# Performance work log

Hardware: AMD Instinct MI355X
Metric: run time of the kernel (lower is better)

The kernel has to match this reference:

```python
import jax, jax.numpy as jnp
import numpy as np

D_MODEL = 2048
N_HEADS = 16
HEAD_DIM = D_MODEL // N_HEADS


def setup_inputs() -> dict:
    key = jax.random.key(0)
    ks = jax.random.split(key, 6)
    B, T = 4, 2048
    scale = 1.0 / np.sqrt(D_MODEL)
    x = jax.random.normal(ks[0], (B, T, D_MODEL), dtype=jnp.float32)
    wq = jax.random.normal(ks[1], (D_MODEL, D_MODEL), dtype=jnp.float32) * scale
    wk = jax.random.normal(ks[2], (D_MODEL, D_MODEL), dtype=jnp.float32) * scale
    wv = jax.random.normal(ks[3], (D_MODEL, D_MODEL), dtype=jnp.float32) * scale
    wo = jax.random.normal(ks[4], (D_MODEL, D_MODEL), dtype=jnp.float32) * scale
    bo = jnp.zeros((D_MODEL,), dtype=jnp.float32)
    return {"x": x, "wq": wq, "wk": wk, "wv": wv, "wo": wo, "bo": bo}


def reference(x, wq, wk, wv, wo, bo):
    B, T, C = x.shape
    H, Dh = N_HEADS, HEAD_DIM
    # torch nn.Linear: y = x @ W.T
    q = (x @ wq.T).reshape(B, T, H, Dh).transpose(0, 2, 1, 3)  # (B,H,T,Dh)
    k = (x @ wk.T).reshape(B, T, H, Dh).transpose(0, 2, 1, 3)
    v = (x @ wv.T).reshape(B, T, H, Dh).transpose(0, 2, 1, 3)
    scores = jnp.einsum('bhqd,bhkd->bhqk', q, k) / np.sqrt(Dh).astype(np.float32)
    attn = jax.nn.softmax(scores, axis=-1)  # no causal mask in source
    out = jnp.einsum('bhqk,bhkd->bhqd', attn, v)
    out = out.transpose(0, 2, 1, 3).reshape(B, T, C)
    return out @ wo.T + bo
```

## Files before the change

kernel.cpp:

```cpp
#include <hip/hip_runtime.h>
#include <hip/hip_bf16.h>
#include <math.h>

typedef __attribute__((ext_vector_type(8))) __bf16 bf16x8;
typedef __attribute__((ext_vector_type(4))) float floatx4;

__device__ inline unsigned short f2u(float f) {
  __hip_bfloat16 h = __float2bfloat16(f);
  unsigned short u;
  __builtin_memcpy(&u, &h, 2);
  return u;
}

__device__ inline floatx4 mfma16(bf16x8 a, bf16x8 b, floatx4 c) {
  return __builtin_amdgcn_mfma_f32_16x16x32_bf16(a, b, c, 0, 0, 0);
}

__device__ inline void gload_lds16(const unsigned short* g, unsigned short* l) {
  __builtin_amdgcn_global_load_lds(
      (__attribute__((address_space(1))) void*)g,
      (__attribute__((address_space(3))) void*)l,
      16, 0, 0);
}

__global__ __launch_bounds__(256) void castk(const float* __restrict__ in,
                                             unsigned short* __restrict__ out,
                                             int n4, float scale) {
  int i = blockIdx.x * 256 + threadIdx.x;
  if (i >= n4) return;
  const float4 v = reinterpret_cast<const float4*>(in)[i];
  ushort4 o;
  o.x = f2u(v.x * scale);
  o.y = f2u(v.y * scale);
  o.z = f2u(v.z * scale);
  o.w = f2u(v.w * scale);
  reinterpret_cast<ushort4*>(out)[i] = o;
}

__global__ __launch_bounds__(256) void castw4(const float* __restrict__ wq,
                                              const float* __restrict__ wk,
                                              const float* __restrict__ wv,
                                              const float* __restrict__ wo,
                                              unsigned short* __restrict__ oq,
                                              unsigned short* __restrict__ ok,
                                              unsigned short* __restrict__ ov,
                                              unsigned short* __restrict__ oo,
                                              float qscale) {
  const int tensor = blockIdx.x >> 12;
  const int i = (blockIdx.x & 4095) * 256 + threadIdx.x;
  const float* in = tensor == 0 ? wq : tensor == 1 ? wk : tensor == 2 ? wv : wo;
  unsigned short* out = tensor == 0 ? oq : tensor == 1 ? ok : tensor == 2 ? ov : oo;
  const float s = tensor == 0 ? qscale : 1.0f;
  const float4 v = reinterpret_cast<const float4*>(in)[i];
  ushort4 o;
  o.x = f2u(v.x * s);
  o.y = f2u(v.y * s);
  o.z = f2u(v.z * s);
  o.w = f2u(v.w * s);
  reinterpret_cast<ushort4*>(out)[i] = o;
}

template <int OUT>
__global__ __launch_bounds__(512, 2)
void gemm256(const unsigned short* __restrict__ A,
             const unsigned short* __restrict__ B,
             unsigned short* __restrict__ Cb,
             float* __restrict__ Cf,
             const float* __restrict__ bias,
             int M, int N, int K) {
  extern __shared__ unsigned short lds[];
  const int t = threadIdx.x;
  const int w = t >> 6;
  const int l = t & 63;
  const int wm = w >> 2;
  const int wn = w & 3;
  const int fr = l & 15;
  const int fkb = l >> 4;
  const int key = fr & 7;
  const int sslot = (l & 7) ^ (l >> 3);

  const int m0 = blockIdx.y * 256;
  const int n0 = blockIdx.x * 256;
  const int T = K >> 6;

  auto stage = [&](const unsigned short* G, int rb, int kt2, int h, int ldsbase) {
    const int d2 = kt2 & 1;
    const int rt = h * 128 + w * 16 + (l >> 3);
    const unsigned short* s0 = G + (size_t)(rb + rt) * K + kt2 * 64 + sslot * 8;
    unsigned short* dst = lds + ldsbase + d2 * 16384 + h * 8192 + w * 1024;
    gload_lds16(s0, dst);
    gload_lds16(s0 + (size_t)8 * K, dst + 512);
  };

  floatx4 acc[8][4];
#pragma unroll
  for (int m = 0; m < 8; m++)
#pragma unroll
    for (int n = 0; n < 4; n++) acc[m][n] = (floatx4){0.f, 0.f, 0.f, 0.f};

  stage(A, m0, 0, 0, 0);
  stage(A, m0, 0, 1, 0);
  stage(B, n0, 0, 0, 32768);
  stage(B, n0, 0, 1, 32768);
  if (1 < T) {
    stage(B, n0, 1, 0, 32768);
    stage(B, n0, 1, 1, 32768);
    asm volatile("s_waitcnt vmcnt(4)" ::: "memory");
  } else {
    asm volatile("s_waitcnt vmcnt(0)" ::: "memory");
  }
  __builtin_amdgcn_s_barrier();

#define GPHASE(q, STAGE_STMT)                                               \
  {                                                                         \
    bf16x8 a00 = *reinterpret_cast<const bf16x8*>(                          \
        Ab + (wm * 128 + (2 * (q)) * 16 + fr) * 64 + ((fkb ^ key)) * 8);    \
    bf16x8 a01 = *reinterpret_cast<const bf16x8*>(                          \
        Ab + (wm * 128 + (2 * (q)) * 16 + fr) * 64 + (((4 + fkb) ^ key)) * 8); \
    bf16x8 a10 = *reinterpret_cast<const bf16x8*>(                          \
        Ab + (wm * 128 + (2 * (q) + 1) * 16 + fr) * 64 + ((fkb ^ key)) * 8);\
    bf16x8 a11 = *reinterpret_cast<const bf16x8*>(                          \
        Ab + (wm * 128 + (2 * (q) + 1) * 16 + fr) * 64 + (((4 + fkb) ^ key)) * 8); \
    STAGE_STMT;                                                             \
    __builtin_amdgcn_s_barrier();                                           \
    asm volatile("s_waitcnt lgkmcnt(0)");                                   \
    __builtin_amdgcn_s_setprio(1);                                          \
    _Pragma("unroll")                                                       \
    for (int n = 0; n < 4; n++) {                                           \
      acc[2 * (q)][n] = mfma16(a00, bfr[0][n], acc[2 * (q)][n]);            \
      acc[2 * (q)][n] = mfma16(a01, bfr[1][n], acc[2 * (q)][n]);            \
      acc[2 * (q) + 1][n] = mfma16(a10, bfr[0][n], acc[2 * (q) + 1][n]);    \
      acc[2 * (q) + 1][n] = mfma16(a11, bfr[1][n], acc[2 * (q) + 1][n]);    \
    }                                                                       \
    __builtin_amdgcn_s_setprio(0);                                          \
    __builtin_amdgcn_s_barrier();                                           \
  }

  for (int kt = 0; kt < T; ++kt) {
    const int d = kt & 1;
    const unsigned short* Ab = lds + d * 16384;
    const unsigned short* Bb = lds + 32768 + d * 16384;

    bf16x8 bfr[2][4];
#pragma unroll
    for (int kk = 0; kk < 2; kk++)
#pragma unroll
      for (int n = 0; n < 4; n++)
        bfr[kk][n] = *reinterpret_cast<const bf16x8*>(
            Bb + (wn * 64 + n * 16 + fr) * 64 + (((kk * 4 + fkb) ^ key)) * 8);

    GPHASE(0, if (kt + 1 < T) stage(A, m0, kt + 1, 0, 0));
    GPHASE(1, if (kt + 1 < T) stage(A, m0, kt + 1, 1, 0));
    GPHASE(2, if (kt + 2 < T) stage(B, n0, kt + 2, 0, 32768));
    GPHASE(3, {
      if (kt + 2 < T) {
        stage(B, n0, kt + 2, 1, 32768);
        asm volatile("s_waitcnt vmcnt(4)" ::: "memory");
      } else {
        asm volatile("s_waitcnt vmcnt(0)" ::: "memory");
      }
    });
  }
#undef GPHASE

  const int er = (l >> 4) * 4;
  const int ec = l & 15;
#pragma unroll
  for (int m = 0; m < 8; m++) {
#pragma unroll
    for (int n = 0; n < 4; n++) {
      const int col = n0 + wn * 64 + n * 16 + ec;
      if (OUT == 2) {
        const int hv = col >> 7, dh = col & 127;
        const int row0 = m0 + wm * 128 + m * 16 + er;
        const int bb = row0 >> 11;
        const int t0 = row0 & 2047;
        unsigned short* vp =
            Cb + (((size_t)(bb * 16 + hv)) * 128 + dh) * 2048 + t0;
#pragma unroll
        for (int r = 0; r < 4; r++) vp[r] = f2u(acc[m][n][r]);
      } else {
#pragma unroll
        for (int r = 0; r < 4; r++) {
          const int row = m0 + wm * 128 + m * 16 + er + r;
          if (OUT == 1) {
            Cf[(size_t)row * N + col] = acc[m][n][r] + bias[col];
          } else {
            Cb[(size_t)row * N + col] = f2u(acc[m][n][r]);
          }
        }
      }
    }
  }
}

__global__ __launch_bounds__(256, 2)
void attn_kernel(const unsigned short* __restrict__ Y2,
                 const unsigned short* __restrict__ Vtg,
                 unsigned short* __restrict__ att) {
  __shared__ unsigned short Kt[64 * 128];
  __shared__ unsigned short Vt[128 * 64];
  __shared__ unsigned short Pl[4][32 * 72];

  const int t = threadIdx.x;
  const int w = t >> 6;
  const int l = t & 63;
  const int bid = blockIdx.x;
  const int bh = bid & 63;
  const int qt = bid >> 6;
  const int b = bh >> 4;
  const int h = bh & 15;

  const size_t ybase = (size_t)b * 2048 * 4096 + (size_t)h * 128;
  const unsigned short* Qp = Y2 + ybase;
  const unsigned short* Kp = Y2 + ybase + 2048;
  const unsigned short* Vp = Vtg + (size_t)bh * 128 * 2048;

  const int fr = l & 15;
  const int fkb = l >> 4;
  const int key = fr & 7;

  const int ksr = t >> 4;
  const int ksl = (t & 15) ^ (ksr & 7);
  const unsigned short* Ksrc = Kp + (size_t)ksr * 4096 + ksl * 8;

  const int vsr = t >> 3;
  const int vsl = (t & 7) ^ (vsr & 7);
  const unsigned short* Vsrc = Vp + (size_t)vsr * 2048 + vsl * 8;

  bf16x8 qf[2][4];
#pragma unroll
  for (int i = 0; i < 2; i++)
#pragma unroll
    for (int kk = 0; kk < 4; kk++)
      qf[i][kk] = *reinterpret_cast<const bf16x8*>(
          &Qp[(size_t)(qt * 128 + w * 32 + i * 16 + fr) * 4096 + kk * 32 + fkb * 8]);

  floatx4 oacc[2][8];
#pragma unroll
  for (int i = 0; i < 2; i++)
#pragma unroll
    for (int nt = 0; nt < 8; nt++) oacc[i][nt] = (floatx4){0.f, 0.f, 0.f, 0.f};
  float mrun[2][4], lrun[2][4];
#pragma unroll
  for (int i = 0; i < 2; i++)
#pragma unroll
    for (int r = 0; r < 4; r++) {
      mrun[i][r] = -INFINITY;
      lrun[i][r] = 0.f;
    }

  unsigned short* Pw = &Pl[w][0];

#pragma unroll
  for (int c = 0; c < 4; c++)
    gload_lds16(Ksrc + (size_t)c * 16 * 4096, &Kt[c * 2048 + w * 512]);
#pragma unroll
  for (int c = 0; c < 4; c++)
    gload_lds16(Vsrc + (size_t)c * 32 * 2048, &Vt[c * 2048 + w * 512]);
  __syncthreads();

  for (int kv = 0; kv < 2048; kv += 64) {
    floatx4 sacc[2][4];
#pragma unroll
    for (int i = 0; i < 2; i++)
#pragma unroll
      for (int nt = 0; nt < 4; nt++) sacc[i][nt] = (floatx4){0.f, 0.f, 0.f, 0.f};
#pragma unroll
    for (int nt = 0; nt < 4; nt++) {
#pragma unroll
      for (int kk = 0; kk < 4; kk++) {
        bf16x8 kf = *reinterpret_cast<const bf16x8*>(
            &Kt[((nt * 16 + fr) * 16 + ((kk * 4 + fkb) ^ key)) * 8]);
        sacc[0][nt] = mfma16(qf[0][kk], kf, sacc[0][nt]);
        sacc[1][nt] = mfma16(qf[1][kk], kf, sacc[1][nt]);
      }
    }

#pragma unroll
    for (int i = 0; i < 2; i++) {
#pragma unroll
      for (int r = 0; r < 4; r++) {
        float s0 = sacc[i][0][r], s1 = sacc[i][1][r];
        float s2 = sacc[i][2][r], s3 = sacc[i][3][r];
        float mx = fmaxf(fmaxf(s0, s1), fmaxf(s2, s3));
        mx = fmaxf(mx, __shfl_xor(mx, 1));
        mx = fmaxf(mx, __shfl_xor(mx, 2));
        mx = fmaxf(mx, __shfl_xor(mx, 4));
        mx = fmaxf(mx, __shfl_xor(mx, 8));
        if (mx > mrun[i][r] + 8.0f) {
          float alpha = __expf(mrun[i][r] - mx);
          mrun[i][r] = mx;
          lrun[i][r] *= alpha;
#pragma unroll
          for (int nt = 0; nt < 8; nt++) oacc[i][nt][r] *= alpha;
        }
        const float m = mrun[i][r];
        float p0 = __expf(s0 - m);
        float p1 = __expf(s1 - m);
        float p2 = __expf(s2 - m);
        float p3 = __expf(s3 - m);
        float ps = (p0 + p1) + (p2 + p3);
        ps += __shfl_xor(ps, 1);
        ps += __shfl_xor(ps, 2);
        ps += __shfl_xor(ps, 4);
        ps += __shfl_xor(ps, 8);
        lrun[i][r] += ps;
        const int pr = i * 16 + fkb * 4 + r;
        Pw[pr * 72 + fr] = f2u(p0);
        Pw[pr * 72 + 16 + fr] = f2u(p1);
        Pw[pr * 72 + 32 + fr] = f2u(p2);
        Pw[pr * 72 + 48 + fr] = f2u(p3);
      }
    }

    __syncthreads();

    if (kv + 64 < 2048) {
#pragma unroll
      for (int c = 0; c < 4; c++)
        gload_lds16(Ksrc + (size_t)(kv + 64 + c * 16) * 4096,
                    &Kt[c * 2048 + w * 512]);
    }

    bf16x8 pf[2][2];
#pragma unroll
    for (int i = 0; i < 2; i++) {
      pf[i][0] = *reinterpret_cast<const bf16x8*>(&Pw[(i * 16 + fr) * 72 + fkb * 8]);
      pf[i][1] = *reinterpret_cast<const bf16x8*>(&Pw[(i * 16 + fr) * 72 + 32 + fkb * 8]);
    }
#pragma unroll
    for (int nt = 0; nt < 8; nt++) {
      const unsigned short* vr = &Vt[(nt * 16 + fr) * 64];
      bf16x8 vf0 = *reinterpret_cast<const bf16x8*>(vr + (fkb ^ key) * 8);
      bf16x8 vf1 = *reinterpret_cast<const bf16x8*>(vr + ((fkb + 4) ^ key) * 8);
#pragma unroll
      for (int i = 0; i < 2; i++) {
        oacc[i][nt] = mfma16(pf[i][0], vf0, oacc[i][nt]);
        oacc[i][nt] = mfma16(pf[i][1], vf1, oacc[i][nt]);
      }
    }

    __syncthreads();

    if (kv + 64 < 2048) {
#pragma unroll
      for (int c = 0; c < 4; c++)
        gload_lds16(Vsrc + (size_t)c * 32 * 2048 + (kv + 64),
                    &Vt[c * 2048 + w * 512]);
    }
  }

#pragma unroll
  for (int i = 0; i < 2; i++) {
#pragma unroll
    for (int r = 0; r < 4; r++) {
      const float inv = 1.0f / lrun[i][r];
      const int row = qt * 128 + w * 32 + i * 16 + fkb * 4 + r;
      unsigned short* op = att + ((size_t)b * 2048 + row) * 2048 + h * 128 + fr;
#pragma unroll
      for (int nt = 0; nt < 8; nt++) op[nt * 16] = f2u(oacc[i][nt][r] * inv);
    }
  }
}

extern "C" void kernel_launch(void* const* d_in, const int* in_sizes, int n_in,
                              void* d_out, int out_size, void* d_ws, size_t ws_size,
                              hipStream_t stream) {
  const float* x = (const float*)d_in[0];
  const float* wq = (const float*)d_in[1];
  const float* wk = (const float*)d_in[2];
  const float* wv = (const float*)d_in[3];
  const float* wo = (const float*)d_in[4];
  const float* bo = (const float*)d_in[5];

  unsigned short* ws = (unsigned short*)d_ws;
  unsigned short* x16 = ws;
  unsigned short* wqkv16 = x16 + 16777216;
  unsigned short* wo16 = wqkv16 + 12582912;
  unsigned short* Y2 = wo16 + 4194304;
  unsigned short* Vtg = Y2 + 33554432;
  unsigned short* att16 = Vtg + 16777216;

  const float sscale = 0.08838834764831845f;

  hipFuncSetAttribute(reinterpret_cast<const void*>(gemm256<0>),
                      hipFuncAttributeMaxDynamicSharedMemorySize, 131072);
  hipFuncSetAttribute(reinterpret_cast<const void*>(gemm256<1>),
                      hipFuncAttributeMaxDynamicSharedMemorySize, 131072);
  hipFuncSetAttribute(reinterpret_cast<const void*>(gemm256<2>),
                      hipFuncAttributeMaxDynamicSharedMemorySize, 131072);

  castk<<<16384, 256, 0, stream>>>(x, x16, 4194304, 1.0f);
  castw4<<<16384, 256, 0, stream>>>(wq, wk, wv, wo,
                                    wqkv16, wqkv16 + 4194304,
                                    wqkv16 + 8388608, wo16, sscale);

  dim3 gqk(16, 32);
  gemm256<0><<<gqk, 512, 131072, stream>>>(x16, wqkv16, Y2, nullptr, nullptr,
                                           8192, 4096, 2048);
  dim3 gv(8, 32);
  gemm256<2><<<gv, 512, 131072, stream>>>(x16, wqkv16 + 8388608, Vtg, nullptr,
                                          nullptr, 8192, 2048, 2048);

  attn_kernel<<<1024, 256, 0, stream>>>(Y2, Vtg, att16);

  dim3 go(8, 32);
  gemm256<1><<<go, 512, 131072, stream>>>(att16, wo16, nullptr, (float*)d_out,
                                          bo, 8192, 2048, 2048);
}
```

Baseline: 542.0 us.

## Enlarge attention blocks to 8 waves and streamline online softmax with exp2

The attention kernel now runs 512-thread blocks, each covering 256 query rows. Each K/V tile staged in LDS therefore serves twice as many queries, and LDS moves to dynamic shared memory. The softmax switches to exp2 by folding log2(e) into the Q weight scale. Rescaling becomes a wave-uniform lazy check, and the per-row sum cross-lane reduction is deferred to the epilogue, cutting shuffles and exp calls per tile. The tighter launch bounds (512,4) may cap registers per thread and cause spills, and the larger block halves the grid size.

Result: slower. 920.7 us (+69.9%).

```diff
diff --git a/kernel.cpp b/kernel.cpp
--- a/kernel.cpp
+++ b/kernel.cpp
@@ -194,13 +194,14 @@
   }
 }
 
-__global__ __launch_bounds__(256, 2)
+__global__ __launch_bounds__(512, 4)
 void attn_kernel(const unsigned short* __restrict__ Y2,
                  const unsigned short* __restrict__ Vtg,
                  unsigned short* __restrict__ att) {
-  __shared__ unsigned short Kt[64 * 128];
-  __shared__ unsigned short Vt[128 * 64];
-  __shared__ unsigned short Pl[4][32 * 72];
+  extern __shared__ unsigned short smem[];
+  unsigned short* Kt = smem;
+  unsigned short* Vt = smem + 8192;
+  unsigned short* Pw = smem + 16384 + (threadIdx.x >> 6) * 2304;
 
   const int t = threadIdx.x;
   const int w = t >> 6;
@@ -223,7 +224,6 @@
   const int ksr = t >> 4;
   const int ksl = (t & 15) ^ (ksr & 7);
   const unsigned short* Ksrc = Kp + (size_t)ksr * 4096 + ksl * 8;
-
   const int vsr = t >> 3;
   const int vsl = (t & 7) ^ (vsr & 7);
   const unsigned short* Vsrc = Vp + (size_t)vsr * 2048 + vsl * 8;
@@ -234,30 +234,28 @@
 #pragma unroll
     for (int kk = 0; kk < 4; kk++)
       qf[i][kk] = *reinterpret_cast<const bf16x8*>(
-          &Qp[(size_t)(qt * 128 + w * 32 + i * 16 + fr) * 4096 + kk * 32 + fkb * 8]);
+          &Qp[(size_t)(qt * 256 + w * 32 + i * 16 + fr) * 4096 + kk * 32 + fkb * 8]);
 
   floatx4 oacc[2][8];
 #pragma unroll
   for (int i = 0; i < 2; i++)
 #pragma unroll
     for (int nt = 0; nt < 8; nt++) oacc[i][nt] = (floatx4){0.f, 0.f, 0.f, 0.f};
-  float mrun[2][4], lrun[2][4];
+  float mrun[2][4], lsum[2][4];
 #pragma unroll
   for (int i = 0; i < 2; i++)
 #pragma unroll
     for (int r = 0; r < 4; r++) {
       mrun[i][r] = -INFINITY;
-      lrun[i][r] = 0.f;
-    }
-
-  unsigned short* Pw = &Pl[w][0];
-
-#pragma unroll
-  for (int c = 0; c < 4; c++)
-    gload_lds16(Ksrc + (size_t)c * 16 * 4096, &Kt[c * 2048 + w * 512]);
-#pragma unroll
-  for (int c = 0; c < 4; c++)
-    gload_lds16(Vsrc + (size_t)c * 32 * 2048, &Vt[c * 2048 + w * 512]);
+      lsum[i][r] = 0.f;
+    }
+
+#pragma unroll
+  for (int c = 0; c < 2; c++)
+    gload_lds16(Ksrc + (size_t)c * 32 * 4096, &Kt[c * 4096 + w * 512]);
+#pragma unroll
+  for (int c = 0; c < 2; c++)
+    gload_lds16(Vsrc + (size_t)c * 64 * 2048, &Vt[c * 4096 + w * 512]);
   __syncthreads();
 
   for (int kv = 0; kv < 2048; kv += 64) {
@@ -277,50 +275,58 @@
       }
     }
 
-#pragma unroll
-    for (int i = 0; i < 2; i++) {
+    float mx4[2][4];
+    float dmax = -INFINITY;
+#pragma unroll
+    for (int i = 0; i < 2; i++)
 #pragma unroll
       for (int r = 0; r < 4; r++) {
-        float s0 = sacc[i][0][r], s1 = sacc[i][1][r];
-        float s2 = sacc[i][2][r], s3 = sacc[i][3][r];
-        float mx = fmaxf(fmaxf(s0, s1), fmaxf(s2, s3));
-        mx = fmaxf(mx, __shfl_xor(mx, 1));
-        mx = fmaxf(mx, __shfl_xor(mx, 2));
-        mx = fmaxf(mx, __shfl_xor(mx, 4));
-        mx = fmaxf(mx, __shfl_xor(mx, 8));
-        if (mx > mrun[i][r] + 8.0f) {
-          float alpha = __expf(mrun[i][r] - mx);
-          mrun[i][r] = mx;
-          lrun[i][r] *= alpha;
+        mx4[i][r] = fmaxf(fmaxf(sacc[i][0][r], sacc[i][1][r]),
+                          fmaxf(sacc[i][2][r], sacc[i][3][r]));
+        dmax = fmaxf(dmax, mx4[i][r] - mrun[i][r]);
+      }
+    if (__any(dmax > 11.5f)) {
+#pragma unroll
+      for (int i = 0; i < 2; i++)
+#pragma unroll
+        for (int r = 0; r < 4; r++) {
+          float mx = mx4[i][r];
+          mx = fmaxf(mx, __shfl_xor(mx, 1));
+          mx = fmaxf(mx, __shfl_xor(mx, 2));
+          mx = fmaxf(mx, __shfl_xor(mx, 4));
+          mx = fmaxf(mx, __shfl_xor(mx, 8));
+          const float mn = fmaxf(mrun[i][r], mx);
+          const float alpha = exp2f(mrun[i][r] - mn);
+          mrun[i][r] = mn;
+          lsum[i][r] *= alpha;
 #pragma unroll
           for (int nt = 0; nt < 8; nt++) oacc[i][nt][r] *= alpha;
         }
+    }
+#pragma unroll
+    for (int i = 0; i < 2; i++)
+#pragma unroll
+      for (int r = 0; r < 4; r++) {
         const float m = mrun[i][r];
-        float p0 = __expf(s0 - m);
-        float p1 = __expf(s1 - m);
-        float p2 = __expf(s2 - m);
-        float p3 = __expf(s3 - m);
-        float ps = (p0 + p1) + (p2 + p3);
-        ps += __shfl_xor(ps, 1);
-        ps += __shfl_xor(ps, 2);
-        ps += __shfl_xor(ps, 4);
-        ps += __shfl_xor(ps, 8);
-        lrun[i][r] += ps;
+        const float p0 = exp2f(sacc[i][0][r] - m);
+        const float p1 = exp2f(sacc[i][1][r] - m);
+        const float p2 = exp2f(sacc[i][2][r] - m);
+        const float p3 = exp2f(sacc[i][3][r] - m);
+        lsum[i][r] += (p0 + p1) + (p2 + p3);
         const int pr = i * 16 + fkb * 4 + r;
         Pw[pr * 72 + fr] = f2u(p0);
         Pw[pr * 72 + 16 + fr] = f2u(p1);
         Pw[pr * 72 + 32 + fr] = f2u(p2);
         Pw[pr * 72 + 48 + fr] = f2u(p3);
       }
-    }
 
     __syncthreads();
 
     if (kv + 64 < 2048) {
 #pragma unroll
-      for (int c = 0; c < 4; c++)
-        gload_lds16(Ksrc + (size_t)(kv + 64 + c * 16) * 4096,
-                    &Kt[c * 2048 + w * 512]);
+      for (int c = 0; c < 2; c++)
+        gload_lds16(Ksrc + (size_t)(kv + 64 + c * 32) * 4096,
+                    &Kt[c * 4096 + w * 512]);
     }
 
     bf16x8 pf[2][2];
@@ -345,9 +351,9 @@
 
     if (kv + 64 < 2048) {
 #pragma unroll
-      for (int c = 0; c < 4; c++)
-        gload_lds16(Vsrc + (size_t)c * 32 * 2048 + (kv + 64),
-                    &Vt[c * 2048 + w * 512]);
+      for (int c = 0; c < 2; c++)
+        gload_lds16(Vsrc + (size_t)c * 64 * 2048 + (kv + 64),
+                    &Vt[c * 4096 + w * 512]);
     }
   }
 
@@ -355,8 +361,13 @@
   for (int i = 0; i < 2; i++) {
 #pragma unroll
     for (int r = 0; r < 4; r++) {
-      const float inv = 1.0f / lrun[i][r];
-      const int row = qt * 128 + w * 32 + i * 16 + fkb * 4 + r;
+      float s = lsum[i][r];
+      s += __shfl_xor(s, 1);
+      s += __shfl_xor(s, 2);
+      s += __shfl_xor(s, 4);
+      s += __shfl_xor(s, 8);
+      const float inv = 1.0f / s;
+      const int row = qt * 256 + w * 32 + i * 16 + fkb * 4 + r;
       unsigned short* op = att + ((size_t)b * 2048 + row) * 2048 + h * 128 + fr;
 #pragma unroll
       for (int nt = 0; nt < 8; nt++) op[nt * 16] = f2u(oacc[i][nt][r] * inv);
@@ -382,7 +393,7 @@
   unsigned short* Vtg = Y2 + 33554432;
   unsigned short* att16 = Vtg + 16777216;
 
-  const float sscale = 0.08838834764831845f;
+  const float sscale = 0.12751744900765256f;
 
   hipFuncSetAttribute(reinterpret_cast<const void*>(gemm256<0>),
                       hipFuncAttributeMaxDynamicSharedMemorySize, 131072);
@@ -390,6 +401,8 @@
                       hipFuncAttributeMaxDynamicSharedMemorySize, 131072);
   hipFuncSetAttribute(reinterpret_cast<const void*>(gemm256<2>),
                       hipFuncAttributeMaxDynamicSharedMemorySize, 131072);
+  hipFuncSetAttribute(reinterpret_cast<const void*>(attn_kernel),
+                      hipFuncAttributeMaxDynamicSharedMemorySize, 69632);
 
   castk<<<16384, 256, 0, stream>>>(x, x16, 4194304, 1.0f);
   castw4<<<16384, 256, 0, stream>>>(wq, wk, wv, wo,
@@ -403,7 +416,7 @@
   gemm256<2><<<gv, 512, 131072, stream>>>(x16, wqkv16 + 8388608, Vtg, nullptr,
                                           nullptr, 8192, 2048, 2048);
 
-  attn_kernel<<<1024, 256, 0, stream>>>(Y2, Vtg, att16);
+  attn_kernel<<<512, 512, 69632, stream>>>(Y2, Vtg, att16);
 
   dim3 go(8, 32);
   gemm256<1><<<go, 512, 131072, stream>>>(att16, wo16, nullptr, (float*)d_out,
```
